# Performance work log

Measured on AMD Instinct MI355X. Metric: run time of the kernel, lower is better.

Reference implementation:

```python
import math
import jax, jax.numpy as jnp
import numpy as np

B, T, C = 8, 1024, 768
H = 12
D = C // H  # 64


def setup_inputs() -> dict:
    key = jax.random.key(0)
    k1, k2, k3, k4, k5 = jax.random.split(key, 5)
    s = 0.02
    return {
        "x": jax.random.normal(k1, (B, T, C), dtype=jnp.float32),
        "w_qkv": jax.random.normal(k2, (C, 3 * C), dtype=jnp.float32) * s,
        "b_qkv": jax.random.normal(k3, (3 * C,), dtype=jnp.float32) * s,
        "w_proj": jax.random.normal(k4, (C, C), dtype=jnp.float32) * s,
        "b_proj": jax.random.normal(k5, (C,), dtype=jnp.float32) * s,
    }


def reference(x, w_qkv, b_qkv, w_proj, b_proj):
    b, t, c = x.shape
    qkv = x @ w_qkv + b_qkv                      # [B,T,3C]
    q, k, v = jnp.split(qkv, 3, axis=-1)
    # [B,T,C] -> [B,H,T,D]
    q = q.reshape(b, t, H, D).transpose(0, 2, 1, 3)
    k = k.reshape(b, t, H, D).transpose(0, 2, 1, 3)
    v = v.reshape(b, t, H, D).transpose(0, 2, 1, 3)
    scale = 1.0 / math.sqrt(D)
    att = jnp.einsum("bhqd,bhkd->bhqk", q, k) * scale   # [B,H,T,T]
    causal = jnp.tril(jnp.ones((t, t), dtype=bool))
    att = jnp.where(causal, att, -jnp.inf)
    att = jax.nn.softmax(att, axis=-1)
    y = jnp.einsum("bhqk,bhkd->bhqd", att, v)            # [B,H,T,D]
    y = y.transpose(0, 2, 1, 3).reshape(b, t, c)
    return y @ w_proj + b_proj
```

## Files before the change

### kernel.cpp

```cpp
#include <hip/hip_runtime.h>
#include <math.h>

#define B_ 8
#define T_ 1024
#define C_ 768
#define H_ 12
#define D_ 64

typedef __bf16 bf16x8 __attribute__((ext_vector_type(8)));
typedef float  f32x4  __attribute__((ext_vector_type(4)));
typedef unsigned short us8 __attribute__((ext_vector_type(8)));
typedef unsigned int   u32x4v __attribute__((ext_vector_type(4)));

typedef __attribute__((address_space(3))) void lds_void;
typedef __attribute__((address_space(1))) const void glb_void;

#define KSC 0.18033688011112043f

__device__ __forceinline__ unsigned short f2bf(float f) {
    unsigned int u = __float_as_uint(f);
    u += 0x7fffu + ((u >> 16) & 1u);
    return (unsigned short)(u >> 16);
}

__global__ __launch_bounds__(256)
void prep_w(const float* __restrict__ w_qkv, const float* __restrict__ b_qkv,
            const float* __restrict__ w_proj,
            unsigned short* __restrict__ wqT, unsigned short* __restrict__ wpT,
            float* __restrict__ bqs) {
    __shared__ unsigned short Ts[64][65];
    const int id  = blockIdx.x;
    const int tid = threadIdx.x;
    if (id == 576) {
        for (int i = tid; i < 3 * C_; i += 256)
            bqs[i] = b_qkv[i] * (i < C_ ? KSC : 1.f);
        return;
    }
    const float* W; unsigned short* Wt; int N, nlim, t2;
    if (id < 432) { t2 = id;       W = w_qkv;  Wt = wqT; N = 3 * C_; nlim = C_; }
    else          { t2 = id - 432; W = w_proj; Wt = wpT; N = C_;     nlim = 0;  }
    const int ntiles = N / 64;
    const int n0 = (t2 % ntiles) * 64, k0 = (t2 / ntiles) * 64;
    for (int i = tid; i < 4096; i += 256) {
        int n = i & 63, k = i >> 6;
        float sc = (n0 + n < nlim) ? KSC : 1.f;
        Ts[n][k] = f2bf(W[(size_t)(k0 + k) * N + n0 + n] * sc);
    }
    __syncthreads();
    for (int i = tid; i < 4096; i += 256) {
        int k = i & 63, n = i >> 6;
        Wt[(size_t)(n0 + n) * 768 + k0 + k] = Ts[n][k];
    }
}

template<int A_FP32, int OUT_BF16>
__global__ __launch_bounds__(256, 3)
void gemm_pipe(const float* __restrict__ Af, const unsigned short* __restrict__ A16,
               const unsigned short* __restrict__ Bt, const float* __restrict__ bias,
               void* __restrict__ Cout, int M, int N, int K) {
    __shared__ __align__(16) unsigned short As[8192];
    __shared__ __align__(16) unsigned short Bs[2][8192];

    const int tid  = threadIdx.x;
    const int lane = tid & 63;
    const int c    = lane & 15;
    const int quad = lane >> 4;
    const int wave = tid >> 6;
    const int wm   = (wave >> 1) * 64;
    const int wn   = (wave & 1) * 64;
    const int bm   = blockIdx.x * 128;
    const int bn   = blockIdx.y * 128;

    const float*          aF[4];
    const unsigned short* aH[4];
    int wAddr[4];
#pragma unroll
    for (int p = 0; p < 4; p++) {
        const int Lp = p * 256 + tid;
        const int r  = Lp >> 3;
        const int kc = (Lp ^ r) & 7;
        if (A_FP32) aF[p] = Af  + (size_t)(bm + r) * K + kc * 8;
        else        aH[p] = A16 + (size_t)(bm + r) * K + kc * 8;
        wAddr[p] = Lp * 8;
    }
    const unsigned short* bS[4];
#pragma unroll
    for (int p = 0; p < 4; p++) {
        const int Lp = p * 256 + tid;
        const int L  = Lp ^ ((Lp >> 3) & 7);
        bS[p] = Bt + (size_t)(bn + (L >> 3)) * K + (L & 7) * 8;
    }
    const int wb = (tid & 0xC0) * 8;

    int aoff[4][2], boff[4][2];
#pragma unroll
    for (int i = 0; i < 4; i++)
#pragma unroll
        for (int ks = 0; ks < 2; ks++) {
            const int kcA = (ks * 4 + quad) ^ (c & 7);
            aoff[i][ks] = ((wm + i * 16 + c) * 8 + kcA) * 8;
            boff[i][ks] = ((wn + i * 16 + c) * 8 + kcA) * 8;
        }

    float4 a0[4], a1[4];
    us8    aR[4];
    f32x4 acc[4][4];
#pragma unroll
    for (int i = 0; i < 4; i++)
#pragma unroll
        for (int j = 0; j < 4; j++) acc[i][j] = (f32x4){0.f, 0.f, 0.f, 0.f};

#pragma unroll
    for (int p = 0; p < 4; p++) {
        __builtin_amdgcn_global_load_lds((glb_void*)bS[p],
            (lds_void*)(&Bs[0][0] + p * 2048 + wb), 16, 0, 0);
        bS[p] += 64;
        if (A_FP32) { a0[p] = *(const float4*)aF[p]; a1[p] = *(const float4*)(aF[p] + 4); aF[p] += 64; }
        else        { aR[p] = *(const us8*)aH[p]; aH[p] += 64; }
    }

    const int R = K >> 6;
    for (int r = 0; r < R; r++) {
        __syncthreads();
#pragma unroll
        for (int p = 0; p < 4; p++) {
            us8 w;
            if (A_FP32) {
                w[0] = f2bf(a0[p].x); w[1] = f2bf(a0[p].y);
                w[2] = f2bf(a0[p].z); w[3] = f2bf(a0[p].w);
                w[4] = f2bf(a1[p].x); w[5] = f2bf(a1[p].y);
                w[6] = f2bf(a1[p].z); w[7] = f2bf(a1[p].w);
            } else w = aR[p];
            *(us8*)&As[wAddr[p]] = w;
        }
        __syncthreads();

        if (r + 1 < R) {
#pragma unroll
            for (int p = 0; p < 4; p++) {
                __builtin_amdgcn_global_load_lds((glb_void*)bS[p],
                    (lds_void*)(&Bs[(r + 1) & 1][0] + p * 2048 + wb), 16, 0, 0);
                bS[p] += 64;
                if (A_FP32) { a0[p] = *(const float4*)aF[p]; a1[p] = *(const float4*)(aF[p] + 4); aF[p] += 64; }
                else        { aR[p] = *(const us8*)aH[p]; aH[p] += 64; }
            }
        }

        const unsigned short* bbuf = &Bs[r & 1][0];
#pragma unroll
        for (int ks = 0; ks < 2; ks++) {
            bf16x8 af[4], bfr[4];
#pragma unroll
            for (int i = 0; i < 4; i++)
                af[i] = __builtin_bit_cast(bf16x8, *(const us8*)&As[aoff[i][ks]]);
#pragma unroll
            for (int j = 0; j < 4; j++)
                bfr[j] = __builtin_bit_cast(bf16x8, *(const us8*)&bbuf[boff[j][ks]]);
#pragma unroll
            for (int i = 0; i < 4; i++)
#pragma unroll
                for (int j = 0; j < 4; j++)
                    acc[i][j] = __builtin_amdgcn_mfma_f32_16x16x32_bf16(af[i], bfr[j], acc[i][j], 0, 0, 0);
        }
    }

    float bs[4];
#pragma unroll
    for (int j = 0; j < 4; j++) bs[j] = bias[bn + wn + j * 16 + c];
#pragma unroll
    for (int i = 0; i < 4; i++) {
        const int gm = bm + wm + i * 16 + quad * 4;
#pragma unroll
        for (int r = 0; r < 4; r++) {
            const size_t ro = (size_t)(gm + r) * N;
#pragma unroll
            for (int j = 0; j < 4; j++) {
                const float v = acc[i][j][r] + bs[j];
                const int gn = bn + wn + j * 16 + c;
                if (OUT_BF16) ((unsigned short*)Cout)[ro + gn] = f2bf(v);
                else          ((float*)Cout)[ro + gn] = v;
            }
        }
    }
}

__device__ __forceinline__ int sigmaK(int k) {
    return 16 * (2 * (k >> 5) + ((k >> 2) & 1)) + 4 * ((k >> 3) & 3) + (k & 3);
}

__global__ __launch_bounds__(256, 3)
void attn_mfma(const unsigned short* __restrict__ qkv, unsigned short* __restrict__ y) {
    __shared__ __align__(16) unsigned short Ks[64 * 72];
    __shared__ __align__(16) unsigned int   Vt[64 * 36];

    const int tid  = threadIdx.x;
    const int wave = tid >> 6;
    const int lane = tid & 63;
    const int c    = lane & 15;
    const int quad = lane >> 4;

    const int id = blockIdx.x;
    const int p  = (id >> 3) & 7;
    const int bh = (id >> 6) * 8 + (id & 7);
    const int b  = bh / H_;
    const int h  = bh - b * H_;

    const int qts[2] = {p, 15 - p};
    const int q0s[2] = {p * 64, (15 - p) * 64};

    const int RS = 3 * C_;
    const unsigned short* kbase = qkv + (size_t)b * T_ * RS + C_ + h * D_;
    const unsigned short* vbase = qkv + (size_t)b * T_ * RS + 2 * C_ + h * D_;

    const u32x4v onesu = {0x3F803F80u, 0x3F803F80u, 0x3F803F80u, 0x3F803F80u};
    const bf16x8 onesf = __builtin_bit_cast(bf16x8, onesu);

    bf16x8 qf[2][2];
#pragma unroll
    for (int t = 0; t < 2; t++) {
        const unsigned short* qrow =
            qkv + ((size_t)(b * T_ + q0s[t] + wave * 16 + c)) * RS + h * D_ + quad * 8;
        qf[t][0] = __builtin_bit_cast(bf16x8, *(const us8*)qrow);
        qf[t][1] = __builtin_bit_cast(bf16x8, *(const us8*)(qrow + 32));
    }

    const int kr0 = tid >> 3, kc0 = tid & 7;
    const int sK0 = sigmaK(kr0) * 72 + kc0 * 8;
    const int sK1 = sigmaK(kr0 + 32) * 72 + kc0 * 8;
    const int dg  = tid >> 4, kp0 = tid & 15;

    us8 kA, kB;
    ushort4 vA0, vB0, vA1, vB1;
    {
        kA = *(const us8*)(kbase + (size_t)kr0 * RS + kc0 * 8);
        kB = *(const us8*)(kbase + (size_t)(kr0 + 32) * RS + kc0 * 8);
        const unsigned short* p0 = vbase + (size_t)(2 * kp0) * RS + dg * 4;
        vA0 = *(const ushort4*)p0;  vB0 = *(const ushort4*)(p0 + RS);
        const unsigned short* p1 = vbase + (size_t)(2 * (kp0 + 16)) * RS + dg * 4;
        vA1 = *(const ushort4*)p1;  vB1 = *(const ushort4*)(p1 + RS);
    }

    f32x4 Oa[2][4];
    f32x4 Ol[2];
#pragma unroll
    for (int t = 0; t < 2; t++) {
        Ol[t] = (f32x4){0.f, 0.f, 0.f, 0.f};
#pragma unroll
        for (int d = 0; d < 4; d++) Oa[t][d] = (f32x4){0.f, 0.f, 0.f, 0.f};
    }

    const int ktEnd = qts[1];
    for (int kt = 0; kt <= ktEnd; kt++) {
        __syncthreads();
        *(us8*)&Ks[sK0] = kA;
        *(us8*)&Ks[sK1] = kB;
        {
            unsigned int* v0 = &Vt[(dg * 4) * 36 + kp0];
            v0[0]   = vA0.x | ((unsigned)vB0.x << 16);
            v0[36]  = vA0.y | ((unsigned)vB0.y << 16);
            v0[72]  = vA0.z | ((unsigned)vB0.z << 16);
            v0[108] = vA0.w | ((unsigned)vB0.w << 16);
            unsigned int* v1 = v0 + 16;
            v1[0]   = vA1.x | ((unsigned)vB1.x << 16);
            v1[36]  = vA1.y | ((unsigned)vB1.y << 16);
            v1[72]  = vA1.z | ((unsigned)vB1.z << 16);
            v1[108] = vA1.w | ((unsigned)vB1.w << 16);
        }
        __syncthreads();

        if (kt < ktEnd) {
            const unsigned short* kp = kbase + (size_t)((kt + 1) * 64) * RS;
            kA = *(const us8*)(kp + (size_t)kr0 * RS + kc0 * 8);
            kB = *(const us8*)(kp + (size_t)(kr0 + 32) * RS + kc0 * 8);
            const unsigned short* vp = vbase + (size_t)((kt + 1) * 64) * RS;
            const unsigned short* p0 = vp + (size_t)(2 * kp0) * RS + dg * 4;
            vA0 = *(const ushort4*)p0;  vB0 = *(const ushort4*)(p0 + RS);
            const unsigned short* p1 = vp + (size_t)(2 * (kp0 + 16)) * RS + dg * 4;
            vA1 = *(const ushort4*)p1;  vB1 = *(const ushort4*)(p1 + RS);
        }

        bf16x8 kf[4][2];
#pragma unroll
        for (int nb = 0; nb < 4; nb++) {
#pragma unroll
            for (int ks = 0; ks < 2; ks++)
                kf[nb][ks] = __builtin_bit_cast(bf16x8,
                    *(const us8*)&Ks[(nb * 16 + c) * 72 + quad * 8 + ks * 32]);
        }

#pragma unroll
        for (int t = 0; t < 2; t++) {
            if (kt > qts[t]) continue;
            const bool diag = (kt == qts[t]);
            const bool doHi = !diag || (wave >= 2);
            const int nbmax = diag ? ((wave >= 2) ? 3 : 1) : 3;

            f32x4 sv[4];
#pragma unroll
            for (int nb = 0; nb < 4; nb++) {
                if (nb <= nbmax) {
                    f32x4 z = (f32x4){0.f, 0.f, 0.f, 0.f};
                    z = __builtin_amdgcn_mfma_f32_16x16x32_bf16(kf[nb][0], qf[t][0], z, 0, 0, 0);
                    sv[nb] = __builtin_amdgcn_mfma_f32_16x16x32_bf16(kf[nb][1], qf[t][1], z, 0, 0, 0);
                }
            }
            if (diag) {
                const int qloc = wave * 16 + c;
#pragma unroll
                for (int nb = 0; nb < 4; nb++) {
                    if (nb <= nbmax) {
                        const int kb = 32 * (nb >> 1) + 4 * (nb & 1) + 8 * quad;
#pragma unroll
                        for (int r = 0; r < 4; r++)
                            if (kb + r > qloc) sv[nb][r] = -INFINITY;
                    }
                }
            }

            unsigned int pd[4][2];
#pragma unroll
            for (int nb = 0; nb < 4; nb++) {
                if (nb <= nbmax) {
                    float p0 = __builtin_amdgcn_exp2f(sv[nb][0]);
                    float p1 = __builtin_amdgcn_exp2f(sv[nb][1]);
                    float p2 = __builtin_amdgcn_exp2f(sv[nb][2]);
                    float p3 = __builtin_amdgcn_exp2f(sv[nb][3]);
                    unsigned u0 = __float_as_uint(p0) + 0x8000u;
                    unsigned u1 = __float_as_uint(p1) + 0x8000u;
                    unsigned u2 = __float_as_uint(p2) + 0x8000u;
                    unsigned u3 = __float_as_uint(p3) + 0x8000u;
                    pd[nb][0] = (u0 >> 16) | (u1 & 0xffff0000u);
                    pd[nb][1] = (u2 >> 16) | (u3 & 0xffff0000u);
                } else {
                    pd[nb][0] = 0u; pd[nb][1] = 0u;
                }
            }

            bf16x8 ap0 = __builtin_bit_cast(bf16x8,
                (u32x4v){pd[0][0], pd[0][1], pd[1][0], pd[1][1]});
            bf16x8 ap1 = __builtin_bit_cast(bf16x8,
                (u32x4v){pd[2][0], pd[2][1], pd[3][0], pd[3][1]});

            Ol[t] = __builtin_amdgcn_mfma_f32_16x16x32_bf16(ap0, onesf, Ol[t], 0, 0, 0);
            if (doHi)
                Ol[t] = __builtin_amdgcn_mfma_f32_16x16x32_bf16(ap1, onesf, Ol[t], 0, 0, 0);

#pragma unroll
            for (int dd = 0; dd < 4; dd++) {
                const unsigned int* vrow = &Vt[(dd * 16 + c) * 36 + quad * 4];
                bf16x8 vb0 = __builtin_bit_cast(bf16x8, *(const u32x4v*)vrow);
                Oa[t][dd] = __builtin_amdgcn_mfma_f32_16x16x32_bf16(ap0, vb0, Oa[t][dd], 0, 0, 0);
                if (doHi) {
                    bf16x8 vb1 = __builtin_bit_cast(bf16x8, *(const u32x4v*)(vrow + 16));
                    Oa[t][dd] = __builtin_amdgcn_mfma_f32_16x16x32_bf16(ap1, vb1, Oa[t][dd], 0, 0, 0);
                }
            }
        }
    }

#pragma unroll
    for (int t = 0; t < 2; t++) {
        unsigned short* yrow =
            y + ((size_t)(b * T_ + q0s[t] + wave * 16)) * C_ + h * D_;
#pragma unroll
        for (int r = 0; r < 4; r++) {
            float inv = 1.f / Ol[t][r];
#pragma unroll
            for (int dd = 0; dd < 4; dd++)
                yrow[(size_t)(quad * 4 + r) * C_ + dd * 16 + c] = f2bf(Oa[t][dd][r] * inv);
        }
    }
}

extern "C" void kernel_launch(void* const* d_in, const int* in_sizes, int n_in,
                              void* d_out, int out_size, void* d_ws, size_t ws_size,
                              hipStream_t stream) {
    const float* x      = (const float*)d_in[0];
    const float* w_qkv  = (const float*)d_in[1];
    const float* b_qkv  = (const float*)d_in[2];
    const float* w_proj = (const float*)d_in[3];
    const float* b_proj = (const float*)d_in[4];
    float* out = (float*)d_out;

    unsigned short* wqT  = (unsigned short*)d_ws;
    unsigned short* wpT  = wqT  + (size_t)3 * C_ * C_;
    unsigned short* qkvb = wpT  + (size_t)C_ * C_;
    unsigned short* yb   = qkvb + (size_t)B_ * T_ * 3 * C_;
    float*          bqs  = (float*)(yb + (size_t)B_ * T_ * C_);

    prep_w<<<577, 256, 0, stream>>>(w_qkv, b_qkv, w_proj, wqT, wpT, bqs);

    gemm_pipe<1, 1><<<dim3(B_ * T_ / 128, 3 * C_ / 128), 256, 0, stream>>>(
        x, nullptr, wqT, bqs, qkvb, B_ * T_, 3 * C_, C_);

    attn_mfma<<<8 * B_ * H_, 256, 0, stream>>>(qkvb, yb);

    gemm_pipe<0, 0><<<dim3(B_ * T_ / 128, C_ / 128), 256, 0, stream>>>(
        nullptr, yb, wpT, b_proj, out, B_ * T_, C_, C_);
}
```

Before: 180.8 us.

## Pre-convert x to bf16 and stream both GEMM operands via global_load_lds

Adds a pass in the prep kernel that converts the fp32 input x to bf16 into the y workspace buffer. The GEMM then loads A tiles straight into double-buffered LDS with global_load_lds, like B, instead of staging through registers with an in-loop conversion and an extra barrier. This removes a per-iteration syncthreads and register pressure, but doubles A's LDS use, which drops the occupancy hint from 3 to 2. It also adds a separate pass that reads x in fp32 and writes it back as bf16.

```diff
diff --git a/kernel.cpp b/kernel.cpp
--- a/kernel.cpp
+++ b/kernel.cpp
@@ -24,13 +24,28 @@
 }
 
 __global__ __launch_bounds__(256)
-void prep_w(const float* __restrict__ w_qkv, const float* __restrict__ b_qkv,
+void prep_w(const float* __restrict__ x,
+            const float* __restrict__ w_qkv, const float* __restrict__ b_qkv,
             const float* __restrict__ w_proj,
             unsigned short* __restrict__ wqT, unsigned short* __restrict__ wpT,
-            float* __restrict__ bqs) {
+            float* __restrict__ bqs, unsigned short* __restrict__ xb) {
     __shared__ unsigned short Ts[64][65];
     const int id  = blockIdx.x;
     const int tid = threadIdx.x;
+    if (id >= 577) {
+        const int xid = id - 577;
+        const float4* xi = (const float4*)x;
+        ushort4* xo = (ushort4*)xb;
+#pragma unroll
+        for (int it = 0; it < 6; it++) {
+            const int idx = (xid * 6 + it) * 256 + tid;
+            float4 v = xi[idx];
+            ushort4 o;
+            o.x = f2bf(v.x); o.y = f2bf(v.y); o.z = f2bf(v.z); o.w = f2bf(v.w);
+            xo[idx] = o;
+        }
+        return;
+    }
     if (id == 576) {
         for (int i = tid; i < 3 * C_; i += 256)
             bqs[i] = b_qkv[i] * (i < C_ ? KSC : 1.f);
@@ -53,12 +68,12 @@
     }
 }
 
-template<int A_FP32, int OUT_BF16>
-__global__ __launch_bounds__(256, 3)
-void gemm_pipe(const float* __restrict__ Af, const unsigned short* __restrict__ A16,
+template<int OUT_BF16>
+__global__ __launch_bounds__(256, 2)
+void gemm_pipe(const unsigned short* __restrict__ A16,
                const unsigned short* __restrict__ Bt, const float* __restrict__ bias,
                void* __restrict__ Cout, int M, int N, int K) {
-    __shared__ __align__(16) unsigned short As[8192];
+    __shared__ __align__(16) unsigned short As[2][8192];
     __shared__ __align__(16) unsigned short Bs[2][8192];
 
     const int tid  = threadIdx.x;
@@ -71,24 +86,14 @@
     const int bm   = blockIdx.x * 128;
     const int bn   = blockIdx.y * 128;
 
-    const float*          aF[4];
-    const unsigned short* aH[4];
-    int wAddr[4];
-#pragma unroll
-    for (int p = 0; p < 4; p++) {
-        const int Lp = p * 256 + tid;
-        const int r  = Lp >> 3;
-        const int kc = (Lp ^ r) & 7;
-        if (A_FP32) aF[p] = Af  + (size_t)(bm + r) * K + kc * 8;
-        else        aH[p] = A16 + (size_t)(bm + r) * K + kc * 8;
-        wAddr[p] = Lp * 8;
-    }
+    const unsigned short* aS[4];
     const unsigned short* bS[4];
 #pragma unroll
     for (int p = 0; p < 4; p++) {
         const int Lp = p * 256 + tid;
         const int L  = Lp ^ ((Lp >> 3) & 7);
-        bS[p] = Bt + (size_t)(bn + (L >> 3)) * K + (L & 7) * 8;
+        aS[p] = A16 + (size_t)(bm + (L >> 3)) * K + (L & 7) * 8;
+        bS[p] = Bt  + (size_t)(bn + (L >> 3)) * K + (L & 7) * 8;
     }
     const int wb = (tid & 0xC0) * 8;
 
@@ -102,8 +107,6 @@
             boff[i][ks] = ((wn + i * 16 + c) * 8 + kcA) * 8;
         }
 
-    float4 a0[4], a1[4];
-    us8    aR[4];
     f32x4 acc[4][4];
 #pragma unroll
     for (int i = 0; i < 4; i++)
@@ -112,47 +115,38 @@
 
 #pragma unroll
     for (int p = 0; p < 4; p++) {
+        __builtin_amdgcn_global_load_lds((glb_void*)aS[p],
+            (lds_void*)(&As[0][0] + p * 2048 + wb), 16, 0, 0);
+        aS[p] += 64;
         __builtin_amdgcn_global_load_lds((glb_void*)bS[p],
             (lds_void*)(&Bs[0][0] + p * 2048 + wb), 16, 0, 0);
         bS[p] += 64;
-        if (A_FP32) { a0[p] = *(const float4*)aF[p]; a1[p] = *(const float4*)(aF[p] + 4); aF[p] += 64; }
-        else        { aR[p] = *(const us8*)aH[p]; aH[p] += 64; }
     }
 
     const int R = K >> 6;
     for (int r = 0; r < R; r++) {
         __syncthreads();
-#pragma unroll
-        for (int p = 0; p < 4; p++) {
-            us8 w;
-            if (A_FP32) {
-                w[0] = f2bf(a0[p].x); w[1] = f2bf(a0[p].y);
-                w[2] = f2bf(a0[p].z); w[3] = f2bf(a0[p].w);
-                w[4] = f2bf(a1[p].x); w[5] = f2bf(a1[p].y);
-                w[6] = f2bf(a1[p].z); w[7] = f2bf(a1[p].w);
-            } else w = aR[p];
-            *(us8*)&As[wAddr[p]] = w;
-        }
-        __syncthreads();
 
         if (r + 1 < R) {
 #pragma unroll
             for (int p = 0; p < 4; p++) {
+                __builtin_amdgcn_global_load_lds((glb_void*)aS[p],
+                    (lds_void*)(&As[(r + 1) & 1][0] + p * 2048 + wb), 16, 0, 0);
+                aS[p] += 64;
                 __builtin_amdgcn_global_load_lds((glb_void*)bS[p],
                     (lds_void*)(&Bs[(r + 1) & 1][0] + p * 2048 + wb), 16, 0, 0);
                 bS[p] += 64;
-                if (A_FP32) { a0[p] = *(const float4*)aF[p]; a1[p] = *(const float4*)(aF[p] + 4); aF[p] += 64; }
-                else        { aR[p] = *(const us8*)aH[p]; aH[p] += 64; }
-            }
-        }
-
+            }
+        }
+
+        const unsigned short* abuf = &As[r & 1][0];
         const unsigned short* bbuf = &Bs[r & 1][0];
 #pragma unroll
         for (int ks = 0; ks < 2; ks++) {
             bf16x8 af[4], bfr[4];
 #pragma unroll
             for (int i = 0; i < 4; i++)
-                af[i] = __builtin_bit_cast(bf16x8, *(const us8*)&As[aoff[i][ks]]);
+                af[i] = __builtin_bit_cast(bf16x8, *(const us8*)&abuf[aoff[i][ks]]);
 #pragma unroll
             for (int j = 0; j < 4; j++)
                 bfr[j] = __builtin_bit_cast(bf16x8, *(const us8*)&bbuf[boff[j][ks]]);
@@ -388,13 +382,15 @@
     unsigned short* yb   = qkvb + (size_t)B_ * T_ * 3 * C_;
     float*          bqs  = (float*)(yb + (size_t)B_ * T_ * C_);
 
-    prep_w<<<577, 256, 0, stream>>>(w_qkv, b_qkv, w_proj, wqT, wpT, bqs);
-
-    gemm_pipe<1, 1><<<dim3(B_ * T_ / 128, 3 * C_ / 128), 256, 0, stream>>>(
-        x, nullptr, wqT, bqs, qkvb, B_ * T_, 3 * C_, C_);
+    unsigned short* xb = yb;
+
+    prep_w<<<1601, 256, 0, stream>>>(x, w_qkv, b_qkv, w_proj, wqT, wpT, bqs, xb);
+
+    gemm_pipe<1><<<dim3(B_ * T_ / 128, 3 * C_ / 128), 256, 0, stream>>>(
+        xb, wqT, bqs, qkvb, B_ * T_, 3 * C_, C_);
 
     attn_mfma<<<8 * B_ * H_, 256, 0, stream>>>(qkvb, yb);
 
-    gemm_pipe<0, 0><<<dim3(B_ * T_ / 128, C_ / 128), 256, 0, stream>>>(
-        nullptr, yb, wpT, b_proj, out, B_ * T_, C_, C_);
-}
+    gemm_pipe<0><<<dim3(B_ * T_ / 128, C_ / 128), 256, 0, stream>>>(
+        yb, wpT, b_proj, out, B_ * T_, C_, C_);
+}
```

New measurement: 181.7 us. No clear change (+0.5%).
